# Kernel tuning notes

Measured on AMD Instinct MI355X. Metric: run time of the kernel, lower is better.

The kernel has to match this reference:

```python
import jax, jax.numpy as jnp
import numpy as np

N, B, E, H, G, L = 128, 2, 512, 1024, 50, 3
RBF_RADIUS = 12.0
AVG_LEN = 60.0


def _resmlp(h, Win, bin_, Wh, bh, Wout, bout):
    # input proj + activation, residual hidden blocks, linear head
    h = jax.nn.gelu(h @ Win + bin_, approximate=False)
    for i in range(Wh.shape[0]):  # fixed small number of layers
        h = h + jax.nn.gelu(h @ Wh[i] + bh[i], approximate=False)
    return h @ Wout + bout


def setup_inputs() -> dict:
    key = jax.random.key(0)
    ks = jax.random.split(key, 20)
    s_in = 1.0 / np.sqrt(3 * E)
    s_h = 1.0 / np.sqrt(H)
    s_g = 1.0 / np.sqrt(G)
    return {
        'x': jax.random.normal(ks[0], (N, B, E), jnp.float32),
        'dist': jax.random.uniform(ks[1], (N, N, B), jnp.float32),
        'vec_hat': jax.random.normal(ks[2], (N, N, B, 3), jnp.float32),
        'mask': jnp.ones((B, N), dtype=bool),
        'rbf_W': jax.random.normal(ks[3], (G, E), jnp.float32) * s_g,
        'rbf_b': jnp.zeros((E,), jnp.float32),
        'e_Win': jax.random.normal(ks[4], (3 * E, H), jnp.float32) * s_in,
        'e_bin': jnp.zeros((H,), jnp.float32),
        'e_Wh': jax.random.normal(ks[5], (L, H, H), jnp.float32) * s_h,
        'e_bh': jnp.zeros((L, H), jnp.float32),
        'e_Wout': jax.random.normal(ks[6], (H, 1), jnp.float32) * s_h,
        'e_bout': jnp.zeros((1,), jnp.float32),
        'f_Win': jax.random.normal(ks[7], (3 * E, H), jnp.float32) * s_in,
        'f_bin': jnp.zeros((H,), jnp.float32),
        'f_Wh': jax.random.normal(ks[8], (L, H, H), jnp.float32) * s_h,
        'f_bh': jnp.zeros((L, H), jnp.float32),
        'f_Wout': jax.random.normal(ks[9], (H, 1), jnp.float32) * s_h,
        'f_bout': jnp.zeros((1,), jnp.float32),
    }


def reference(x, dist, vec_hat, mask, rbf_W, rbf_b, e_Win, e_bin, e_Wh, e_bh,
              e_Wout, e_bout, f_Win, f_bin, f_Wh, f_bh, f_Wout, f_bout):
    # Gaussian RBF expansion + linear projection to embed_dim
    offset = jnp.linspace(0.0, RBF_RADIUS, G)
    coeff = -0.5 / (offset[1] - offset[0]) ** 2
    g = jnp.exp(coeff * (dist[..., None] - offset) ** 2)       # (N,N,B,G)
    rbf = g @ rbf_W + rbf_b                                    # (N,N,B,E)

    # all-pairs concat feature: [x_i, x_j, rbf_ij]  -> (N,N,B,3E)
    feat = jnp.concatenate([
        jnp.broadcast_to(x[:, None], rbf.shape),
        jnp.broadcast_to(x[None, :], rbf.shape),
        rbf,
    ], axis=-1)

    entries = (mask.T[:, None] & mask.T[None, :])[..., None].astype(feat.dtype)  # (N,N,B,1)

    energy_pairs = _resmlp(feat, e_Win, e_bin, e_Wh, e_bh, e_Wout, e_bout)       # (N,N,B,1)
    force_pairs = _resmlp(feat, f_Win, f_bin, f_Wh, f_bh, f_Wout, f_bout) * vec_hat  # (N,N,B,3)

    energy = (energy_pairs * entries).sum((0, 1)) / AVG_LEN ** 2  # (B,1)
    forces = (force_pairs * entries).sum(0) / AVG_LEN             # (N,B,3)
    # torch: forces.transpose(0,1)[mask]; mask is all-True here, so this is a reshape
    forces = jnp.swapaxes(forces, 0, 1).reshape(-1, 3)            # (B*N,3)
    return energy, forces
```

## Files before the change

kernel.cpp:

```cpp
#include <hip/hip_runtime.h>
#include <stdint.h>

typedef __bf16 bf16x8 __attribute__((ext_vector_type(8)));
typedef __bf16 bf16x4 __attribute__((ext_vector_type(4)));
typedef float  f32x4  __attribute__((ext_vector_type(4)));
typedef unsigned int u32;

__device__ __forceinline__ void gl_lds16(const void* gptr, void* lptr) {
    __builtin_amdgcn_global_load_lds(
        (const __attribute__((address_space(1))) u32*)gptr,
        (__attribute__((address_space(3))) u32*)lptr,
        16, 0, 0);
}

__device__ __forceinline__ float gelu_f(float x) {
    float u = 0.7978845608f * x * (1.0f + 0.044715f * x * x);
    float e = __expf(2.0f * u);
    float t = 1.0f - 2.0f / (e + 1.0f);
    return 0.5f * x * (1.0f + t);
}

#define MEMFENCE __asm__ __volatile__("" ::: "memory")

__global__ __launch_bounds__(256)
void prep_all(const float* __restrict__ dist, __bf16* __restrict__ G,
              const float* __restrict__ x, __bf16* __restrict__ xb,
              const float* __restrict__ rbfW, const float* __restrict__ rbf_b,
              __bf16* __restrict__ M1, float* __restrict__ out) {
    const int b = blockIdx.x;
    const int t = threadIdx.x;
    if (b < 1024) {
        const int row = b * 32 + (t >> 3);
        const int c0 = (t & 7) * 8;
        const float sp = 12.0f / 49.0f;
        const float coeff = -0.5f / (sp * sp);
        const float d = dist[row];
        bf16x8 v;
#pragma unroll
        for (int q = 0; q < 8; ++q) {
            const int k = c0 + q;
            float val;
            if (k < 50)       { float tt = d - (float)k * sp; val = __expf(coeff * tt * tt); }
            else if (k == 50) val = 1.0f;
            else              val = 0.0f;
            v[q] = (__bf16)val;
        }
        *(bf16x8*)(G + (size_t)row * 64 + c0) = v;
    } else if (b < 1152) {
        const int idx = (b - 1024) * 256 + t;
        float4 v = *(const float4*)(x + idx * 4);
        bf16x4 o;
        o[0] = (__bf16)v.x; o[1] = (__bf16)v.y; o[2] = (__bf16)v.z; o[3] = (__bf16)v.w;
        *(bf16x4*)(xb + idx * 4) = o;
    } else if (b < 1280) {
        const int tt = (b - 1152) * 256 + t;
        const int r = tt >> 8;
        const int c = (tt & 255) * 2;
        float v0 = 0.f, v1 = 0.f;
        if (r < 50)       { v0 = rbfW[r * 512 + c]; v1 = rbfW[r * 512 + c + 1]; }
        else if (r == 50) { v0 = rbf_b[c];          v1 = rbf_b[c + 1]; }
        M1[r * 512 + c] = (__bf16)v0;
        M1[r * 512 + c + 1] = (__bf16)v1;
    } else {
        const int i = (b - 1280) * 256 + t;
        if (i < 770) out[i] = 0.0f;
    }
}

__global__ __launch_bounds__(256)
void transpose_all(const float* __restrict__ eWin, const float* __restrict__ fWin,
                   __bf16* __restrict__ eWinT, __bf16* __restrict__ fWinT,
                   const float* __restrict__ eWh, const float* __restrict__ fWh,
                   __bf16* __restrict__ eWhT, __bf16* __restrict__ fWhT) {
    const int z = blockIdx.z;
    int K, branch, l;
    const float* src;
    __bf16* dst;
    if (z < 2) {
        K = 1536; branch = z; l = 0;
        src = branch ? fWin : eWin;
        dst = branch ? fWinT : eWinT;
    } else {
        K = 1024; const int zz = z - 2; branch = zz / 3; l = zz - branch * 3;
        src = (branch ? fWh : eWh) + (size_t)l * 1024 * 1024;
        dst = (branch ? fWhT : eWhT) + (size_t)l * 1024 * 1024;
    }
    const int Ncols = 1024;
    const int bk = blockIdx.x * 64;
    if (bk >= K) return;
    const int bn = blockIdx.y * 64;

    __shared__ float tile[64][65];
    const int tid = threadIdx.x;
    const int tr = tid >> 4;
    const int tc = (tid & 15) * 4;
#pragma unroll
    for (int p = 0; p < 4; ++p) {
        const int r = tr + p * 16;
        float4 v = *(const float4*)&src[(size_t)(bk + r) * Ncols + bn + tc];
        tile[r][tc] = v.x; tile[r][tc + 1] = v.y;
        tile[r][tc + 2] = v.z; tile[r][tc + 3] = v.w;
    }
    __syncthreads();
#pragma unroll
    for (int p = 0; p < 4; ++p) {
        const int rn = tr + p * 16;
        bf16x4 o;
        o[0] = (__bf16)tile[tc + 0][rn];
        o[1] = (__bf16)tile[tc + 1][rn];
        o[2] = (__bf16)tile[tc + 2][rn];
        o[3] = (__bf16)tile[tc + 3][rn];
        *(bf16x4*)&dst[(size_t)(bn + rn) * K + bk + tc] = o;
    }
}

template <int NK, int NBN, int MODE, bool DUAL, int MINW, bool SWZ>
__global__ __launch_bounds__(256, MINW)
void gemm_k(const __bf16* __restrict__ A0, const __bf16* __restrict__ A1,
            const __bf16* __restrict__ B0, const __bf16* __restrict__ B1,
            int lda, int ldb, int ldc,
            const float* __restrict__ bias0, const float* __restrict__ bias1,
            __bf16* __restrict__ C0, __bf16* __restrict__ C1,
            float* __restrict__ Cf0, float* __restrict__ Cf1,
            const float* __restrict__ P0, const float* __restrict__ P1,
            const float* __restrict__ wout0, const float* __restrict__ wout1,
            float* __restrict__ dot0, float* __restrict__ dot1) {
    constexpr int NBS = (NBN == 16) ? 4 : (NBN == 8) ? 3 : 0;
    __shared__ __align__(16) __bf16 As[3][128 * 32];
    __shared__ __align__(16) __bf16 Bs[3][128 * 32];

    const int tid = threadIdx.x;
    int bn, bm, branch = 0;
    if constexpr (SWZ) {
        const int x = blockIdx.x & 7;
        const int slot = blockIdx.x >> 3;
        bn = slot & (NBN - 1);
        int grp = x + ((slot >> NBS) << 3);
        if constexpr (DUAL) {
            const int half = (gridDim.x >> NBS) >> 1;
            branch = (grp >= half);
            if (branch) grp -= half;
        }
        bm = grp;
    } else {
        int f2 = blockIdx.x;
        if constexpr (DUAL) {
            const int half = gridDim.x >> 1;
            branch = (f2 >= half);
            if (branch) f2 -= half;
        }
        bn = f2 & (NBN - 1);
        bm = f2 >> NBS;
    }
    const int w = tid >> 6;
    const int lane = tid & 63;

    const __bf16* Ab = (DUAL && branch) ? A1 : A0;
    const __bf16* Bb = (DUAL && branch) ? B1 : B0;

    const int r0 = tid >> 2;
    const int s0 = tid & 3;
    const char* gA0 = (const char*)Ab + (size_t)(bm * 128 + r0) * lda + s0 * 16;
    const char* gA1 = gA0 + (size_t)64 * lda;
    const char* gB0 = (const char*)Bb + (size_t)(bn * 128 + r0) * ldb + s0 * 16;
    const char* gB1 = gB0 + (size_t)64 * ldb;

    char* lA0 = (char*)&As[0][0] + w * 1024;
    char* lA1 = (char*)&As[1][0] + w * 1024;
    char* lA2 = (char*)&As[2][0] + w * 1024;
    char* lB0 = (char*)&Bs[0][0] + w * 1024;
    char* lB1 = (char*)&Bs[1][0] + w * 1024;
    char* lB2 = (char*)&Bs[2][0] + w * 1024;

    const int wm = (w >> 1) & 1;
    const int wn = w & 1;
    const int lm = lane & 15;
    const int ko = (lane >> 4) << 3;
    const int fo = (wm * 64 + lm) * 32 + ko;
    const int go = (wn * 64 + lm) * 32 + ko;
    const __bf16* pA0 = &As[0][0] + fo;
    const __bf16* pA1 = &As[1][0] + fo;
    const __bf16* pA2 = &As[2][0] + fo;
    const __bf16* pB0 = &Bs[0][0] + go;
    const __bf16* pB1 = &Bs[1][0] + go;
    const __bf16* pB2 = &Bs[2][0] + go;

    f32x4 acc[4][4];
    const f32x4 zero = {0.0f, 0.0f, 0.0f, 0.0f};
#pragma unroll
    for (int i = 0; i < 4; ++i)
#pragma unroll
        for (int j = 0; j < 4; ++j) acc[i][j] = zero;

    auto stage = [&](int buf) {
        char* la = (buf == 0) ? lA0 : (buf == 1) ? lA1 : lA2;
        char* lb = (buf == 0) ? lB0 : (buf == 1) ? lB1 : lB2;
        gl_lds16(gA0, la); gl_lds16(gA1, la + 4096);
        gl_lds16(gB0, lb); gl_lds16(gB1, lb + 4096);
        gA0 += 64; gA1 += 64; gB0 += 64; gB1 += 64;
    };
    auto compute = [&](int buf) {
        const __bf16* pa = (buf == 0) ? pA0 : (buf == 1) ? pA1 : pA2;
        const __bf16* pb = (buf == 0) ? pB0 : (buf == 1) ? pB1 : pB2;
        bf16x8 af[4], bfg[4];
#pragma unroll
        for (int i = 0; i < 4; ++i) {
            af[i]  = *(const bf16x8*)(pa + i * 512);
            bfg[i] = *(const bf16x8*)(pb + i * 512);
        }
#pragma unroll
        for (int mi = 0; mi < 4; ++mi)
#pragma unroll
            for (int ni = 0; ni < 4; ++ni)
                acc[mi][ni] = __builtin_amdgcn_mfma_f32_16x16x32_bf16(
                    af[mi], bfg[ni], acc[mi][ni], 0, 0, 0);
    };
    auto iterstep = [&](int cbuf, int sbuf) {
        MEMFENCE;
        __builtin_amdgcn_s_waitcnt(0xF74);
        __builtin_amdgcn_s_barrier();
        MEMFENCE;
        compute(cbuf);
        MEMFENCE;
        stage(sbuf);
        MEMFENCE;
    };

    stage(0);
    stage(1);
    constexpr int NIT = NK - 2;
    constexpr int NG = NIT / 3;
    constexpr int NR = NIT % 3;
    for (int g = 0; g < NG; ++g) {
        iterstep(0, 2);
        iterstep(1, 0);
        iterstep(2, 1);
    }
    if constexpr (NR >= 1) iterstep(0, 2);
    if constexpr (NR >= 2) iterstep(1, 0);
    MEMFENCE;
    __builtin_amdgcn_s_waitcnt(0xF74);
    __builtin_amdgcn_s_barrier();
    MEMFENCE;
    compute((NK - 2) % 3);
    MEMFENCE;
    __builtin_amdgcn_s_waitcnt(0xF70);
    __builtin_amdgcn_s_barrier();
    MEMFENCE;
    compute((NK - 1) % 3);

    const int col0 = bn * 128 + wn * 64 + lm;
    const int row0 = bm * 128 + wm * 64 + ((lane >> 4) << 2);
    const int ldaE = lda >> 1;

    float rowdot[16];
    if constexpr (MODE == 1) {
#pragma unroll
        for (int q = 0; q < 16; ++q) rowdot[q] = 0.0f;
    }

    const bool side = (MODE == 2) && (bn >= 8);
    const float* bp = (MODE == 2) ? (side ? bias1 : bias0)
                                  : ((DUAL && branch) ? bias1 : bias0);
    __bf16* Cout = (MODE == 2) ? (side ? C1 : C0)
                               : ((DUAL && branch) ? C1 : C0);
    const float* woutb = (MODE == 1) ? ((DUAL && branch) ? wout1 : wout0) : nullptr;

#pragma unroll
    for (int ni = 0; ni < 4; ++ni) {
        const int gn = col0 + ni * 16;
        const int gnl = (MODE == 2) ? (gn & 1023) : gn;
        float bv = 0.0f;
        if constexpr (MODE <= 2) bv = bp[gnl];
        float wv = 0.0f;
        if constexpr (MODE == 1) wv = woutb[gn];

        float res[16];
        if constexpr (MODE == 0 || MODE == 1) {
#pragma unroll
            for (int mi = 0; mi < 4; ++mi)
#pragma unroll
                for (int rr = 0; rr < 4; ++rr)
                    res[mi * 4 + rr] =
                        (float)Ab[(size_t)(row0 + mi * 16 + rr) * ldaE + gn];
        } else if constexpr (MODE == 2) {
#pragma unroll
            for (int mi = 0; mi < 4; ++mi)
#pragma unroll
                for (int rr = 0; rr < 4; ++rr) {
                    const int gm = row0 + mi * 16 + rr;
                    const int p0row = ((gm >> 8) << 1) | (gm & 1);
                    const int p1row = gm & 255;
                    res[mi * 4 + rr] = P0[(size_t)p0row * 2048 + gn]
                                     + P1[(size_t)p1row * 2048 + gn];
                }
        }
        MEMFENCE;

#pragma unroll
        for (int mi = 0; mi < 4; ++mi) {
#pragma unroll
            for (int rr = 0; rr < 4; ++rr) {
                const int gm = row0 + mi * 16 + rr;
                const float a = acc[mi][ni][rr];
                if constexpr (MODE == 0) {
                    float v = gelu_f(a + bv) + res[mi * 4 + rr];
                    Cout[(size_t)gm * ldc + gn] = (__bf16)v;
                } else if constexpr (MODE == 1) {
                    float v = gelu_f(a + bv) + res[mi * 4 + rr];
                    rowdot[mi * 4 + rr] += v * wv;
                } else if constexpr (MODE == 2) {
                    float v = a + bv + res[mi * 4 + rr];
                    Cout[(size_t)gm * ldc + gnl] = (__bf16)gelu_f(v);
                } else if constexpr (MODE == 3) {
                    float* Cfw = (DUAL && branch) ? Cf1 : Cf0;
                    Cfw[(size_t)gm * ldc + gn] = a;
                } else {
                    C0[(size_t)gm * ldc + gn] = (__bf16)a;
                }
            }
        }
    }

    if constexpr (MODE == 1) {
#pragma unroll
        for (int s = 1; s < 16; s <<= 1)
#pragma unroll
            for (int q = 0; q < 16; ++q) rowdot[q] += __shfl_xor(rowdot[q], s);
        if (lm == 0) {
            float* dotb = (DUAL && branch) ? dot1 : dot0;
            float* dp = dotb + (size_t)(bn * 2 + wn) * 32768 + row0;
#pragma unroll
            for (int q = 0; q < 16; ++q)
                dp[(q >> 2) * 16 + (q & 3)] = rowdot[q];
        }
    }
}

#define WBAR(imm) do { MEMFENCE; __builtin_amdgcn_s_waitcnt(imm); \
                       __builtin_amdgcn_s_barrier(); MEMFENCE; } while (0)

template <int MODE, bool DUAL, int NBN, int NT, int LDA, int LDB, bool PIPE2>
__global__ __launch_bounds__(512, 2)
void gemm256(const __bf16* __restrict__ A0, const __bf16* __restrict__ A1,
             const __bf16* __restrict__ B0, const __bf16* __restrict__ B1,
             const float* __restrict__ bias0, const float* __restrict__ bias1,
             __bf16* __restrict__ C0, __bf16* __restrict__ C1,
             const float* __restrict__ wout0, const float* __restrict__ wout1,
             float* __restrict__ dot0, float* __restrict__ dot1,
             const float* __restrict__ P0, const float* __restrict__ P1) {
    constexpr int NBUF = PIPE2 ? 2 : ((NT >= 3) ? 4 : 2);
    constexpr int NBS = (NBN == 8) ? 3 : 2;
    __shared__ __align__(16) char ldsbuf[NBUF * 32768];

    const int tid = threadIdx.x;
    const int nxg = gridDim.x >> 3;
    const int id = (blockIdx.x & 7) * nxg + (blockIdx.x >> 3);
    const int bn = id & (NBN - 1);
    int rest = id >> NBS;
    int branch = 0;
    if constexpr (DUAL) { branch = rest >> 7; rest &= 127; }
    const int bm = rest;

    const __bf16* __restrict__ Ab = (DUAL && branch) ? A1 : A0;
    const __bf16* __restrict__ Bb = (DUAL && branch) ? B1 : B0;

    const int w = tid >> 6;
    const int lane = tid & 63;

    const int srow = tid >> 2;
    const int scol = ((tid & 3) << 4) ^ (((tid >> 3) & 3) << 4);
    const char* gA = (const char*)Ab + (size_t)(bm * 256 + srow) * LDA + scol;
    const char* gB = (const char*)Bb + (size_t)(bn * 256 + srow) * LDB + scol;

    auto stageA = [&](int kt, int buf) {
        const size_t ko = (size_t)kt * 64;
        char* d = ldsbuf + buf * 32768 + w * 1024;
        gl_lds16(gA + ko,             d);
        gl_lds16(gA + ko + 128 * LDA, d + 8192);
    };
    auto stageB = [&](int kt, int buf) {
        const size_t ko = (size_t)kt * 64;
        char* d = ldsbuf + buf * 32768 + w * 1024;
        gl_lds16(gB + ko,             d + 16384);
        gl_lds16(gB + ko + 128 * LDB, d + 24576);
    };

    const int wm = w >> 2, wn = w & 3;
    const int lm = lane & 15, lq = lane >> 4;
    const int swz = ((lm >> 1) & 3) << 4;
    const int rA = (wm * 128 + lm) * 64 + ((lq * 16) ^ swz);
    const int rB = 16384 + (wn * 64 + lm) * 64 + ((lq * 16) ^ swz);

    f32x4 acc[4][8];
    const f32x4 zero = {0.0f, 0.0f, 0.0f, 0.0f};
#pragma unroll
    for (int i = 0; i < 4; ++i)
#pragma unroll
        for (int j = 0; j < 8; ++j) acc[i][j] = zero;

    auto body = [&](int kt, int cbuf, int sbuf, bool dostage) {
        const char* Lb = ldsbuf + cbuf * 32768;
        MEMFENCE;
        bf16x8 a[8], b[4];
#pragma unroll
        for (int ni = 0; ni < 4; ++ni)
            b[ni] = *(const bf16x8*)(Lb + rB + ni * 1024);
#pragma unroll
        for (int mi = 0; mi < 4; ++mi)
            a[mi] = *(const bf16x8*)(Lb + rA + mi * 1024);
        if (dostage) stageA(kt + 3, sbuf);
        MEMFENCE;
        __builtin_amdgcn_s_waitcnt(0xC07F);
        MEMFENCE;
        __builtin_amdgcn_s_setprio(1);
#pragma unroll
        for (int ni = 0; ni < 4; ++ni)
#pragma unroll
            for (int mi = 0; mi < 4; ++mi)
                acc[ni][mi] = __builtin_amdgcn_mfma_f32_16x16x32_bf16(
                    b[ni], a[mi], acc[ni][mi], 0, 0, 0);
        __builtin_amdgcn_s_setprio(0);
        __builtin_amdgcn_s_barrier();
        MEMFENCE;
#pragma unroll
        for (int mi = 4; mi < 8; ++mi)
            a[mi] = *(const bf16x8*)(Lb + rA + mi * 1024);
        if (dostage) stageB(kt + 3, sbuf);
        MEMFENCE;
        __builtin_amdgcn_s_waitcnt(0xC07F);
        MEMFENCE;
        __builtin_amdgcn_s_setprio(1);
#pragma unroll
        for (int ni = 0; ni < 4; ++ni)
#pragma unroll
            for (int mi = 4; mi < 8; ++mi)
                acc[ni][mi] = __builtin_amdgcn_mfma_f32_16x16x32_bf16(
                    b[ni], a[mi], acc[ni][mi], 0, 0, 0);
        __builtin_amdgcn_s_setprio(0);
    };

    auto body2 = [&](int kt, int buf, bool dostage) {
        const char* Lb = ldsbuf + buf * 32768;
        MEMFENCE;
        bf16x8 a[8], b[4];
#pragma unroll
        for (int ni = 0; ni < 4; ++ni)
            b[ni] = *(const bf16x8*)(Lb + rB + ni * 1024);
#pragma unroll
        for (int mi = 0; mi < 8; ++mi)
            a[mi] = *(const bf16x8*)(Lb + rA + mi * 1024);
        MEMFENCE;
        __builtin_amdgcn_s_waitcnt(0xC07F);
        MEMFENCE;
        __builtin_amdgcn_s_barrier();
        MEMFENCE;
        if (dostage) { stageA(kt + 2, buf); stageB(kt + 2, buf); }
        MEMFENCE;
        __builtin_amdgcn_s_setprio(1);
#pragma unroll
        for (int ni = 0; ni < 4; ++ni)
#pragma unroll
            for (int mi = 0; mi < 8; ++mi)
                acc[ni][mi] = __builtin_amdgcn_mfma_f32_16x16x32_bf16(
                    b[ni], a[mi], acc[ni][mi], 0, 0, 0);
        __builtin_amdgcn_s_setprio(0);
    };

    if constexpr (NT == 32 && !PIPE2) {
        stageA(0, 0); stageB(0, 0);
        stageA(1, 1); stageB(1, 1);
        stageA(2, 2); stageB(2, 2);
        for (int g = 0; g < 7; ++g) {
            const int k0 = g * 4;
            WBAR(0xF78); body(k0 + 0, 0, 3, true);
            WBAR(0xF78); body(k0 + 1, 1, 0, true);
            WBAR(0xF78); body(k0 + 2, 2, 1, true);
            WBAR(0xF78); body(k0 + 3, 3, 2, true);
        }
        WBAR(0xF78); body(28, 0, 3, true);
        WBAR(0xF78); body(29, 1, 0, false);
        WBAR(0xF74); body(30, 2, 1, false);
        WBAR(0xF70); body(31, 3, 2, false);
    } else if constexpr (NT == 32 && PIPE2) {
        stageA(0, 0); stageB(0, 0);
        stageA(1, 1); stageB(1, 1);
        for (int g = 0; g < 15; ++g) {
            WBAR(0xF74); body2(2 * g + 0, 0, true);
            WBAR(0xF74); body2(2 * g + 1, 1, true);
        }
        WBAR(0xF74); body2(30, 0, false);
        WBAR(0xF70); body2(31, 1, false);
    } else {
        stageA(0, 0); stageB(0, 0);
        stageA(1, 1); stageB(1, 1);
        WBAR(0xF74); body2(0, 0, false);
        WBAR(0xF70); body2(1, 1, false);
    }

    const int rowb = bm * 256 + wm * 128 + lm;
    const int nbase = bn * 256 + wn * 64 + lq * 4;

    if constexpr (MODE == 2) {
        const bool side = (bn >= (NBN >> 1));
        const float* __restrict__ bp = side ? bias1 : bias0;
        __bf16* __restrict__ Cw = side ? C1 : C0;
        const int nloc = nbase & 1023;
        f32x4 bv[4], p0v[4];
        const size_t p0base = (size_t)((bm << 1) | (lm & 1)) * 2048;
#pragma unroll
        for (int ni = 0; ni < 4; ++ni) {
            bv[ni]  = *(const f32x4*)&bp[nloc + ni * 16];
            p0v[ni] = *(const f32x4*)&P0[p0base + nbase + ni * 16];
        }
#pragma unroll
        for (int mi = 0; mi < 8; ++mi) {
            const int p1row = wm * 128 + mi * 16 + lm;
            f32x4 p1v[4];
#pragma unroll
            for (int ni = 0; ni < 4; ++ni)
                p1v[ni] = *(const f32x4*)&P1[(size_t)p1row * 2048 + nbase + ni * 16];
            MEMFENCE;
            const size_t rb = (size_t)(rowb + mi * 16) * 1024;
#pragma unroll
            for (int ni = 0; ni < 4; ++ni) {
                bf16x4 o;
#pragma unroll
                for (int r = 0; r < 4; ++r)
                    o[r] = (__bf16)gelu_f(acc[ni][mi][r] + bv[ni][r] +
                                          p0v[ni][r] + p1v[ni][r]);
                *(bf16x4*)&Cw[rb + nloc + ni * 16] = o;
            }
        }
        return;
    }

    const float* __restrict__ bp = (DUAL && branch) ? bias1 : bias0;
    f32x4 bv[4];
#pragma unroll
    for (int ni = 0; ni < 4; ++ni)
        bv[ni] = *(const f32x4*)&bp[nbase + ni * 16];

    if constexpr (MODE == 0) {
        __bf16* __restrict__ Cw = (DUAL && branch) ? C1 : C0;
#pragma unroll
        for (int mi = 0; mi < 8; ++mi) {
            const size_t rb = (size_t)(rowb + mi * 16) * 1024;
            bf16x4 res[4];
#pragma unroll
            for (int ni = 0; ni < 4; ++ni)
                res[ni] = *(const bf16x4*)&Ab[rb + nbase + ni * 16];
            MEMFENCE;
#pragma unroll
            for (int ni = 0; ni < 4; ++ni) {
                bf16x4 o;
#pragma unroll
                for (int r = 0; r < 4; ++r)
                    o[r] = (__bf16)(gelu_f(acc[ni][mi][r] + bv[ni][r]) +
                                    (float)res[ni][r]);
                *(bf16x4*)&Cw[rb + nbase + ni * 16] = o;
            }
        }
    } else if constexpr (MODE == 1) {
        const float* __restrict__ wb = (DUAL && branch) ? wout1 : wout0;
        f32x4 wv[4];
#pragma unroll
        for (int ni = 0; ni < 4; ++ni)
            wv[ni] = *(const f32x4*)&wb[nbase + ni * 16];
        float rd[8];
#pragma unroll
        for (int q = 0; q < 8; ++q) rd[q] = 0.0f;
#pragma unroll
        for (int mi = 0; mi < 8; ++mi) {
            const size_t rb = (size_t)(rowb + mi * 16) * 1024;
            bf16x4 res[4];
#pragma unroll
            for (int ni = 0; ni < 4; ++ni)
                res[ni] = *(const bf16x4*)&Ab[rb + nbase + ni * 16];
            MEMFENCE;
#pragma unroll
            for (int ni = 0; ni < 4; ++ni)
#pragma unroll
                for (int r = 0; r < 4; ++r) {
                    float v = gelu_f(acc[ni][mi][r] + bv[ni][r]) +
                              (float)res[ni][r];
                    rd[mi] += v * wv[ni][r];
                }
        }
#pragma unroll
        for (int mi = 0; mi < 8; ++mi) {
            rd[mi] += __shfl_xor(rd[mi], 16);
            rd[mi] += __shfl_xor(rd[mi], 32);
        }
        if (lq == 0) {
            float* __restrict__ db = (DUAL && branch) ? dot1 : dot0;
            float* dp = db + (size_t)(bn * 4 + wn) * 32768 + bm * 256 + wm * 128;
#pragma unroll
            for (int mi = 0; mi < 8; ++mi)
                dp[mi * 16 + lm] = rd[mi];
        }
    }
}

__global__ __launch_bounds__(128)
void finalize(const float* __restrict__ dot_e, const float* __restrict__ dot_f,
              const float* __restrict__ eb, const float* __restrict__ fb,
              const float* __restrict__ vec, float* __restrict__ out) {
    const int bj = blockIdx.x;
    const int bb = bj >> 7, jj = bj & 127;
    const int i = threadIdx.x;
    const int m = (i * 128 + jj) * 2 + bb;
    float e = eb[0], f = fb[0];
#pragma unroll
    for (int s = 0; s < 16; ++s) {
        e += dot_e[(size_t)s * 32768 + m];
        f += dot_f[(size_t)s * 32768 + m];
    }
    f *= (1.0f / 60.0f);
    float fx = f * vec[(size_t)m * 3 + 0];
    float fy = f * vec[(size_t)m * 3 + 1];
    float fz = f * vec[(size_t)m * 3 + 2];
#pragma unroll
    for (int off = 32; off > 0; off >>= 1) {
        e  += __shfl_down(e, off);
        fx += __shfl_down(fx, off);
        fy += __shfl_down(fy, off);
        fz += __shfl_down(fz, off);
    }
    __shared__ float red[2][4];
    const int wv = i >> 6, lane = i & 63;
    if (lane == 0) { red[wv][0] = e; red[wv][1] = fx; red[wv][2] = fy; red[wv][3] = fz; }
    __syncthreads();
    if (i == 0) {
        atomicAdd(&out[bb], (red[0][0] + red[1][0]) * (1.0f / 3600.0f));
        float* fo = out + 2 + bj * 3;
        fo[0] = red[0][1] + red[1][1];
        fo[1] = red[0][2] + red[1][2];
        fo[2] = red[0][3] + red[1][3];
    }
}

extern "C" void kernel_launch(void* const* d_in, const int* in_sizes, int n_in,
                              void* d_out, int out_size, void* d_ws, size_t ws_size,
                              hipStream_t stream) {
    const float* x     = (const float*)d_in[0];
    const float* dist  = (const float*)d_in[1];
    const float* vec   = (const float*)d_in[2];
    const float* rbfW  = (const float*)d_in[4];
    const float* rbf_b = (const float*)d_in[5];
    const float* eWin  = (const float*)d_in[6];
    const float* ebin  = (const float*)d_in[7];
    const float* eWh   = (const float*)d_in[8];
    const float* ebh   = (const float*)d_in[9];
    const float* eWout = (const float*)d_in[10];
    const float* ebout = (const float*)d_in[11];
    const float* fWin  = (const float*)d_in[12];
    const float* fbin  = (const float*)d_in[13];
    const float* fWh   = (const float*)d_in[14];
    const float* fbh   = (const float*)d_in[15];
    const float* fWout = (const float*)d_in[16];
    const float* fbout = (const float*)d_in[17];
    float* out = (float*)d_out;

    char* p = (char*)d_ws;
    __bf16* WinTcat = (__bf16*)p;
    __bf16* eWinT = WinTcat;          p += (size_t)1024 * 1536 * 2;
    __bf16* fWinT = (__bf16*)p;       p += (size_t)1024 * 1536 * 2;
    __bf16* eWhT0 = (__bf16*)p;       p += (size_t)3 * 1024 * 1024 * 2;
    __bf16* fWhT0 = (__bf16*)p;       p += (size_t)3 * 1024 * 1024 * 2;
    __bf16* xb  = (__bf16*)p;         p += (size_t)256 * 512 * 2;
    __bf16* M1  = (__bf16*)p;         p += (size_t)128 * 512 * 2;
    __bf16* WgT = (__bf16*)p;         p += (size_t)2048 * 128 * 2;
    __bf16* G   = (__bf16*)p;         p += (size_t)32768 * 64 * 2;
    float* P0   = (float*)p;          p += (size_t)256 * 2048 * 4;
    float* P1   = (float*)p;          p += (size_t)256 * 2048 * 4;
    float* dot_e = (float*)p;         p += (size_t)16 * 32768 * 4;
    float* dot_f = (float*)p;         p += (size_t)16 * 32768 * 4;
    const size_t SLAB = (size_t)32768 * 1024 * 2;
    __bf16* he0 = (__bf16*)p;         p += SLAB;
    __bf16* hf0 = (__bf16*)p;         p += SLAB;
    __bf16* hA  = (__bf16*)p;         p += SLAB;

    prep_all<<<dim3(1284), dim3(256), 0, stream>>>(
        dist, G, x, xb, rbfW, rbf_b, M1, out);
    transpose_all<<<dim3(24, 16, 8), dim3(256), 0, stream>>>(
        eWin, fWin, eWinT, fWinT, eWh, fWh, eWhT0, fWhT0);

    const dim3 blk(256);
    gemm_k<16, 16, 3, true, 3, false><<<dim3(64), blk, 0, stream>>>(
        xb, xb, WinTcat, WinTcat + 512, 1024, 3072, 2048,
        nullptr, nullptr, nullptr, nullptr, P0, P1,
        nullptr, nullptr, nullptr, nullptr, nullptr, nullptr);
    gemm_k<16, 1, 4, false, 3, false><<<dim3(16), blk, 0, stream>>>(
        WinTcat + 1024, nullptr, M1, nullptr, 3072, 1024, 128,
        nullptr, nullptr, WgT, nullptr, nullptr, nullptr,
        nullptr, nullptr, nullptr, nullptr, nullptr, nullptr);

    const dim3 blk512(512);
    gemm256<2, false, 8, 2, 128, 256, false><<<dim3(1024), blk512, 0, stream>>>(
        G, nullptr, WgT, nullptr, ebin, fbin, he0, hf0,
        nullptr, nullptr, nullptr, nullptr, P0, P1);

    gemm256<0, false, 4, 32, 2048, 2048, true><<<dim3(512), blk512, 0, stream>>>(
        he0, nullptr, eWhT0, nullptr, ebh + 0, nullptr,
        hA, nullptr, nullptr, nullptr, nullptr, nullptr, nullptr, nullptr);
    gemm256<0, false, 4, 32, 2048, 2048, true><<<dim3(512), blk512, 0, stream>>>(
        hA, nullptr, eWhT0 + (size_t)1048576, nullptr, ebh + 1024, nullptr,
        he0, nullptr, nullptr, nullptr, nullptr, nullptr, nullptr, nullptr);
    gemm256<0, false, 4, 32, 2048, 2048, true><<<dim3(512), blk512, 0, stream>>>(
        hf0, nullptr, fWhT0, nullptr, fbh + 0, nullptr,
        hA, nullptr, nullptr, nullptr, nullptr, nullptr, nullptr, nullptr);
    gemm256<0, false, 4, 32, 2048, 2048, true><<<dim3(512), blk512, 0, stream>>>(
        hA, nullptr, fWhT0 + (size_t)1048576, nullptr, fbh + 1024, nullptr,
        hf0, nullptr, nullptr, nullptr, nullptr, nullptr, nullptr, nullptr);
    gemm256<1, true, 4, 32, 2048, 2048, true><<<dim3(1024), blk512, 0, stream>>>(
        he0, hf0, eWhT0 + (size_t)2 * 1048576, fWhT0 + (size_t)2 * 1048576,
        ebh + 2048, fbh + 2048, nullptr, nullptr,
        eWout, fWout, dot_e, dot_f, nullptr, nullptr);

    finalize<<<dim3(256), dim3(128), 0, stream>>>(dot_e, dot_f, ebout, fbout, vec, out);
}
```

Before: 709.2 us.

## Split GEMM kernels: 256-thread first-layer GEMM and 4-buffer pipeline for hidden layers

```diff
diff --git a/kernel.cpp b/kernel.cpp
--- a/kernel.cpp
+++ b/kernel.cpp
@@ -340,8 +340,8 @@
 #define WBAR(imm) do { MEMFENCE; __builtin_amdgcn_s_waitcnt(imm); \
                        __builtin_amdgcn_s_barrier(); MEMFENCE; } while (0)
 
-template <int MODE, bool DUAL, int NBN, int NT, int LDA, int LDB, bool PIPE2>
-__global__ __launch_bounds__(512, 2)
+template <int MODE, bool DUAL, int NBN, int NT, int LDA, int LDB>
+__global__ __launch_bounds__(256, 2)
 void gemm256(const __bf16* __restrict__ A0, const __bf16* __restrict__ A1,
              const __bf16* __restrict__ B0, const __bf16* __restrict__ B1,
              const float* __restrict__ bias0, const float* __restrict__ bias1,
@@ -349,9 +349,8 @@
              const float* __restrict__ wout0, const float* __restrict__ wout1,
              float* __restrict__ dot0, float* __restrict__ dot1,
              const float* __restrict__ P0, const float* __restrict__ P1) {
-    constexpr int NBUF = PIPE2 ? 2 : ((NT >= 3) ? 4 : 2);
-    constexpr int NBS = (NBN == 8) ? 3 : 2;
-    __shared__ __align__(16) char ldsbuf[NBUF * 32768];
+    constexpr int NBS = (NBN == 16) ? 4 : (NBN == 8) ? 3 : 2;
+    __shared__ __align__(16) char ldsbuf[2 * 24576];
 
     const int tid = threadIdx.x;
     const int nxg = gridDim.x >> 3;
@@ -371,19 +370,140 @@
     const int srow = tid >> 2;
     const int scol = ((tid & 3) << 4) ^ (((tid >> 3) & 3) << 4);
     const char* gA = (const char*)Ab + (size_t)(bm * 256 + srow) * LDA + scol;
-    const char* gB = (const char*)Bb + (size_t)(bn * 256 + srow) * LDB + scol;
-
-    auto stageA = [&](int kt, int buf) {
+    const char* gB = (const char*)Bb + (size_t)(bn * 128 + srow) * LDB + scol;
+
+    auto stageT = [&](int kt, int buf) {
+        const size_t ko = (size_t)kt * 64;
+        char* d = ldsbuf + buf * 24576 + w * 1024;
+        gl_lds16(gA + ko,             d);
+        gl_lds16(gA + ko +  64 * LDA, d + 4096);
+        gl_lds16(gA + ko + 128 * LDA, d + 8192);
+        gl_lds16(gA + ko + 192 * LDA, d + 12288);
+        gl_lds16(gB + ko,             d + 16384);
+        gl_lds16(gB + ko +  64 * LDB, d + 20480);
+    };
+
+    const int wm = w >> 1, wn = w & 1;
+    const int lm = lane & 15, lq = lane >> 4;
+    const int swz = ((lm >> 1) & 3) << 4;
+    const int rA = (wm * 128 + lm) * 64 + ((lq * 16) ^ swz);
+    const int rB = 16384 + (wn * 64 + lm) * 64 + ((lq * 16) ^ swz);
+
+    f32x4 acc[4][8];
+    const f32x4 zero = {0.0f, 0.0f, 0.0f, 0.0f};
+#pragma unroll
+    for (int i = 0; i < 4; ++i)
+#pragma unroll
+        for (int j = 0; j < 8; ++j) acc[i][j] = zero;
+
+    auto body2 = [&](int kt, int buf, bool dostage) {
+        const char* Lb = ldsbuf + buf * 24576;
+        MEMFENCE;
+        bf16x8 a[8], b[4];
+#pragma unroll
+        for (int ni = 0; ni < 4; ++ni)
+            b[ni] = *(const bf16x8*)(Lb + rB + ni * 1024);
+#pragma unroll
+        for (int mi = 0; mi < 8; ++mi)
+            a[mi] = *(const bf16x8*)(Lb + rA + mi * 1024);
+        MEMFENCE;
+        __builtin_amdgcn_s_waitcnt(0xC07F);
+        MEMFENCE;
+        __builtin_amdgcn_s_barrier();
+        MEMFENCE;
+        if (dostage) stageT(kt + 2, buf);
+        MEMFENCE;
+        __builtin_amdgcn_s_setprio(1);
+#pragma unroll
+        for (int ni = 0; ni < 4; ++ni)
+#pragma unroll
+            for (int mi = 0; mi < 8; ++mi)
+                acc[ni][mi] = __builtin_amdgcn_mfma_f32_16x16x32_bf16(
+                    b[ni], a[mi], acc[ni][mi], 0, 0, 0);
+        __builtin_amdgcn_s_setprio(0);
+    };
+
+    stageT(0, 0);
+    stageT(1, 1);
+    WBAR(0xF76); body2(0, 0, false);
+    WBAR(0xF70); body2(1, 1, false);
+
+    const int rowb = bm * 256 + wm * 128 + lm;
+    const int nbase = bn * 128 + wn * 64 + lq * 4;
+
+    const bool side = (bn >= (NBN >> 1));
+    const float* __restrict__ bp = side ? bias1 : bias0;
+    __bf16* __restrict__ Cw = side ? C1 : C0;
+    const int nloc = nbase & 1023;
+    f32x4 bv[4], p0v[4];
+    const size_t p0base = (size_t)((bm << 1) | (lm & 1)) * 2048;
+#pragma unroll
+    for (int ni = 0; ni < 4; ++ni) {
+        bv[ni]  = *(const f32x4*)&bp[nloc + ni * 16];
+        p0v[ni] = *(const f32x4*)&P0[p0base + nbase + ni * 16];
+    }
+#pragma unroll
+    for (int mi = 0; mi < 8; ++mi) {
+        const int p1row = wm * 128 + mi * 16 + lm;
+        f32x4 p1v[4];
+#pragma unroll
+        for (int ni = 0; ni < 4; ++ni)
+            p1v[ni] = *(const f32x4*)&P1[(size_t)p1row * 2048 + nbase + ni * 16];
+        MEMFENCE;
+        const size_t rb = (size_t)(rowb + mi * 16) * 1024;
+#pragma unroll
+        for (int ni = 0; ni < 4; ++ni) {
+            bf16x4 o;
+#pragma unroll
+            for (int r = 0; r < 4; ++r)
+                o[r] = (__bf16)gelu_f(acc[ni][mi][r] + bv[ni][r] +
+                                      p0v[ni][r] + p1v[ni][r]);
+            *(bf16x4*)&Cw[rb + nloc + ni * 16] = o;
+        }
+    }
+}
+
+template <int MODE, bool DUAL>
+__global__ __launch_bounds__(512, 1)
+void gemm8p(const __bf16* __restrict__ A0, const __bf16* __restrict__ A1,
+            const __bf16* __restrict__ B0, const __bf16* __restrict__ B1,
+            const float* __restrict__ bias0, const float* __restrict__ bias1,
+            __bf16* __restrict__ C0, __bf16* __restrict__ C1,
+            const float* __restrict__ wout0, const float* __restrict__ wout1,
+            float* __restrict__ dot0, float* __restrict__ dot1) {
+    __shared__ __align__(16) char ldsbuf[4 * 32768];
+
+    const int tid = threadIdx.x;
+    const int nxg = gridDim.x >> 3;
+    const int id = (blockIdx.x & 7) * nxg + (blockIdx.x >> 3);
+    const int bn = id & 3;
+    int rest = id >> 2;
+    int branch = 0;
+    if constexpr (DUAL) { branch = rest >> 7; rest &= 127; }
+    const int bm = rest;
+
+    const __bf16* __restrict__ Ab = (DUAL && branch) ? A1 : A0;
+    const __bf16* __restrict__ Bb = (DUAL && branch) ? B1 : B0;
+
+    const int w = tid >> 6;
+    const int lane = tid & 63;
+
+    const int srow = tid >> 2;
+    const int scol = ((tid & 3) << 4) ^ (((tid >> 3) & 3) << 4);
+    const char* gA = (const char*)Ab + (size_t)(bm * 256 + srow) * 2048 + scol;
+    const char* gB = (const char*)Bb + (size_t)(bn * 256 + srow) * 2048 + scol;
+
+    auto stageA2 = [&](int kt, int buf) {
         const size_t ko = (size_t)kt * 64;
         char* d = ldsbuf + buf * 32768 + w * 1024;
-        gl_lds16(gA + ko,             d);
-        gl_lds16(gA + ko + 128 * LDA, d + 8192);
+        gl_lds16(gA + ko,              d);
+        gl_lds16(gA + ko + 128 * 2048, d + 8192);
     };
-    auto stageB = [&](int kt, int buf) {
+    auto stageB2 = [&](int kt, int buf) {
         const size_t ko = (size_t)kt * 64;
         char* d = ldsbuf + buf * 32768 + w * 1024;
-        gl_lds16(gB + ko,             d + 16384);
-        gl_lds16(gB + ko + 128 * LDB, d + 24576);
+        gl_lds16(gB + ko,              d + 16384);
+        gl_lds16(gB + ko + 128 * 2048, d + 24576);
     };
 
     const int wm = w >> 2, wn = w & 3;
@@ -401,15 +521,17 @@
 
     auto body = [&](int kt, int cbuf, int sbuf, bool dostage) {
         const char* Lb = ldsbuf + cbuf * 32768;
-        MEMFENCE;
         bf16x8 a[8], b[4];
+        MEMFENCE;
 #pragma unroll
         for (int ni = 0; ni < 4; ++ni)
             b[ni] = *(const bf16x8*)(Lb + rB + ni * 1024);
 #pragma unroll
         for (int mi = 0; mi < 4; ++mi)
             a[mi] = *(const bf16x8*)(Lb + rA + mi * 1024);
-        if (dostage) stageA(kt + 3, sbuf);
+        if (dostage) stageA2(kt + 3, sbuf);
+        MEMFENCE;
+        __builtin_amdgcn_s_barrier();
         MEMFENCE;
         __builtin_amdgcn_s_waitcnt(0xC07F);
         MEMFENCE;
@@ -421,12 +543,15 @@
                 acc[ni][mi] = __builtin_amdgcn_mfma_f32_16x16x32_bf16(
                     b[ni], a[mi], acc[ni][mi], 0, 0, 0);
         __builtin_amdgcn_s_setprio(0);
+        MEMFENCE;
         __builtin_amdgcn_s_barrier();
         MEMFENCE;
 #pragma unroll
         for (int mi = 4; mi < 8; ++mi)
             a[mi] = *(const bf16x8*)(Lb + rA + mi * 1024);
-        if (dostage) stageB(kt + 3, sbuf);
+        if (dostage) stageB2(kt + 3, sbuf);
+        MEMFENCE;
+        __builtin_amdgcn_s_barrier();
         MEMFENCE;
         __builtin_amdgcn_s_waitcnt(0xC07F);
         MEMFENCE;
@@ -440,100 +565,23 @@
         __builtin_amdgcn_s_setprio(0);
     };
 
-    auto body2 = [&](int kt, int buf, bool dostage) {
-        const char* Lb = ldsbuf + buf * 32768;
-        MEMFENCE;
-        bf16x8 a[8], b[4];
-#pragma unroll
-        for (int ni = 0; ni < 4; ++ni)
-            b[ni] = *(const bf16x8*)(Lb + rB + ni * 1024);
-#pragma unroll
-        for (int mi = 0; mi < 8; ++mi)
-            a[mi] = *(const bf16x8*)(Lb + rA + mi * 1024);
-        MEMFENCE;
-        __builtin_amdgcn_s_waitcnt(0xC07F);
-        MEMFENCE;
-        __builtin_amdgcn_s_barrier();
-        MEMFENCE;
-        if (dostage) { stageA(kt + 2, buf); stageB(kt + 2, buf); }
-        MEMFENCE;
-        __builtin_amdgcn_s_setprio(1);
-#pragma unroll
-        for (int ni = 0; ni < 4; ++ni)
-#pragma unroll
-            for (int mi = 0; mi < 8; ++mi)
-                acc[ni][mi] = __builtin_amdgcn_mfma_f32_16x16x32_bf16(
-                    b[ni], a[mi], acc[ni][mi], 0, 0, 0);
-        __builtin_amdgcn_s_setprio(0);
-    };
-
-    if constexpr (NT == 32 && !PIPE2) {
-        stageA(0, 0); stageB(0, 0);
-        stageA(1, 1); stageB(1, 1);
-        stageA(2, 2); stageB(2, 2);
-        for (int g = 0; g < 7; ++g) {
-            const int k0 = g * 4;
-            WBAR(0xF78); body(k0 + 0, 0, 3, true);
-            WBAR(0xF78); body(k0 + 1, 1, 0, true);
-            WBAR(0xF78); body(k0 + 2, 2, 1, true);
-            WBAR(0xF78); body(k0 + 3, 3, 2, true);
-        }
-        WBAR(0xF78); body(28, 0, 3, true);
-        WBAR(0xF78); body(29, 1, 0, false);
-        WBAR(0xF74); body(30, 2, 1, false);
-        WBAR(0xF70); body(31, 3, 2, false);
-    } else if constexpr (NT == 32 && PIPE2) {
-        stageA(0, 0); stageB(0, 0);
-        stageA(1, 1); stageB(1, 1);
-        for (int g = 0; g < 15; ++g) {
-            WBAR(0xF74); body2(2 * g + 0, 0, true);
-            WBAR(0xF74); body2(2 * g + 1, 1, true);
-        }
-        WBAR(0xF74); body2(30, 0, false);
-        WBAR(0xF70); body2(31, 1, false);
-    } else {
-        stageA(0, 0); stageB(0, 0);
-        stageA(1, 1); stageB(1, 1);
-        WBAR(0xF74); body2(0, 0, false);
-        WBAR(0xF70); body2(1, 1, false);
-    }
+    stageA2(0, 0); stageB2(0, 0);
+    stageA2(1, 1); stageB2(1, 1);
+    stageA2(2, 2); stageB2(2, 2);
+    for (int g = 0; g < 7; ++g) {
+        const int k0 = g * 4;
+        WBAR(0xF78); body(k0 + 0, 0, 3, true);
+        WBAR(0xF78); body(k0 + 1, 1, 0, true);
+        WBAR(0xF78); body(k0 + 2, 2, 1, true);
+        WBAR(0xF78); body(k0 + 3, 3, 2, true);
+    }
+    WBAR(0xF78); body(28, 0, 3, true);
+    WBAR(0xF78); body(29, 1, 0, false);
+    WBAR(0xF74); body(30, 2, 1, false);
+    WBAR(0xF70); body(31, 3, 2, false);
 
     const int rowb = bm * 256 + wm * 128 + lm;
     const int nbase = bn * 256 + wn * 64 + lq * 4;
-
-    if constexpr (MODE == 2) {
-        const bool side = (bn >= (NBN >> 1));
-        const float* __restrict__ bp = side ? bias1 : bias0;
-        __bf16* __restrict__ Cw = side ? C1 : C0;
-        const int nloc = nbase & 1023;
-        f32x4 bv[4], p0v[4];
-        const size_t p0base = (size_t)((bm << 1) | (lm & 1)) * 2048;
-#pragma unroll
-        for (int ni = 0; ni < 4; ++ni) {
-            bv[ni]  = *(const f32x4*)&bp[nloc + ni * 16];
-            p0v[ni] = *(const f32x4*)&P0[p0base + nbase + ni * 16];
-        }
-#pragma unroll
-        for (int mi = 0; mi < 8; ++mi) {
-            const int p1row = wm * 128 + mi * 16 + lm;
-            f32x4 p1v[4];
-#pragma unroll
-            for (int ni = 0; ni < 4; ++ni)
-                p1v[ni] = *(const f32x4*)&P1[(size_t)p1row * 2048 + nbase + ni * 16];
-            MEMFENCE;
-            const size_t rb = (size_t)(rowb + mi * 16) * 1024;
-#pragma unroll
-            for (int ni = 0; ni < 4; ++ni) {
-                bf16x4 o;
-#pragma unroll
-                for (int r = 0; r < 4; ++r)
-                    o[r] = (__bf16)gelu_f(acc[ni][mi][r] + bv[ni][r] +
-                                          p0v[ni][r] + p1v[ni][r]);
-                *(bf16x4*)&Cw[rb + nloc + ni * 16] = o;
-            }
-        }
-        return;
-    }
 
     const float* __restrict__ bp = (DUAL && branch) ? bias1 : bias0;
     f32x4 bv[4];
@@ -561,7 +609,7 @@
                 *(bf16x4*)&Cw[rb + nbase + ni * 16] = o;
             }
         }
-    } else if constexpr (MODE == 1) {
+    } else {
         const float* __restrict__ wb = (DUAL && branch) ? wout1 : wout0;
         f32x4 wv[4];
 #pragma unroll
@@ -696,27 +744,27 @@
         nullptr, nullptr, WgT, nullptr, nullptr, nullptr,
         nullptr, nullptr, nullptr, nullptr, nullptr, nullptr);
 
-    const dim3 blk512(512);
-    gemm256<2, false, 8, 2, 128, 256, false><<<dim3(1024), blk512, 0, stream>>>(
+    gemm256<2, false, 16, 2, 128, 256><<<dim3(2048), blk, 0, stream>>>(
         G, nullptr, WgT, nullptr, ebin, fbin, he0, hf0,
         nullptr, nullptr, nullptr, nullptr, P0, P1);
 
-    gemm256<0, false, 4, 32, 2048, 2048, true><<<dim3(512), blk512, 0, stream>>>(
+    const dim3 blk512(512);
+    gemm8p<0, false><<<dim3(512), blk512, 0, stream>>>(
         he0, nullptr, eWhT0, nullptr, ebh + 0, nullptr,
-        hA, nullptr, nullptr, nullptr, nullptr, nullptr, nullptr, nullptr);
-    gemm256<0, false, 4, 32, 2048, 2048, true><<<dim3(512), blk512, 0, stream>>>(
+        hA, nullptr, nullptr, nullptr, nullptr, nullptr);
+    gemm8p<0, false><<<dim3(512), blk512, 0, stream>>>(
         hA, nullptr, eWhT0 + (size_t)1048576, nullptr, ebh + 1024, nullptr,
-        he0, nullptr, nullptr, nullptr, nullptr, nullptr, nullptr, nullptr);
-    gemm256<0, false, 4, 32, 2048, 2048, true><<<dim3(512), blk512, 0, stream>>>(
+        he0, nullptr, nullptr, nullptr, nullptr, nullptr);
+    gemm8p<0, false><<<dim3(512), blk512, 0, stream>>>(
         hf0, nullptr, fWhT0, nullptr, fbh + 0, nullptr,
-        hA, nullptr, nullptr, nullptr, nullptr, nullptr, nullptr, nullptr);
-    gemm256<0, false, 4, 32, 2048, 2048, true><<<dim3(512), blk512, 0, stream>>>(
+        hA, nullptr, nullptr, nullptr, nullptr, nullptr);
+    gemm8p<0, false><<<dim3(512), blk512, 0, stream>>>(
         hA, nullptr, fWhT0 + (size_t)1048576, nullptr, fbh + 1024, nullptr,
-        hf0, nullptr, nullptr, nullptr, nullptr, nullptr, nullptr, nullptr);
-    gemm256<1, true, 4, 32, 2048, 2048, true><<<dim3(1024), blk512, 0, stream>>>(
+        hf0, nullptr, nullptr, nullptr, nullptr, nullptr);
+    gemm8p<1, true><<<dim3(1024), blk512, 0, stream>>>(
         he0, hf0, eWhT0 + (size_t)2 * 1048576, fWhT0 + (size_t)2 * 1048576,
         ebh + 2048, fbh + 2048, nullptr, nullptr,
-        eWout, fWout, dot_e, dot_f, nullptr, nullptr);
+        eWout, fWout, dot_e, dot_f);
 
     finalize<<<dim3(256), dim3(128), 0, stream>>>(dot_e, dot_f, ebout, fbout, vec, out);
 }
```

New measurement: 726.4 us. +2.4%, slower.
